# Kernel tuning notes

Measured on AMD Instinct MI355X. Metric: run time of the kernel, lower is better.

## Reference

```python
import jax, jax.numpy as jnp
import numpy as np

H = 1024        # hidden_size
V = 50257       # output_size (vocab)
L = 2048        # number of encoder annotations


def setup_inputs() -> dict:
    key = jax.random.key(0)
    ks = jax.random.split(key, 24)
    s = 0.02
    inp = {
        "input_tok": jax.random.randint(ks[0], (1,), 0, V),
        "hidden": jax.random.normal(ks[1], (1, H), jnp.float32),
        "encoder_outputs": jax.random.normal(ks[2], (L, 1, 2 * H), jnp.float32),
        "cell_state": jax.random.normal(ks[3], (1, H), jnp.float32),
        # embedding: Linear(V, H)
        "W_emb": jax.random.normal(ks[4], (V, H), jnp.float32) * s,
        "b_emb": jnp.zeros((H,), jnp.float32),
        # attn_layer: Linear(3H, H); attn_output: Linear(H, 1)
        "W_attn": jax.random.normal(ks[5], (3 * H, H), jnp.float32) * s,
        "b_attn": jnp.zeros((H,), jnp.float32),
        "W_attn_out": jax.random.normal(ks[6], (H, 1), jnp.float32) * s,
        "b_attn_out": jnp.zeros((1,), jnp.float32),
        # LSTM gates: Linear(3H + H, H) each
        "W_i": jax.random.normal(ks[7], (4 * H, H), jnp.float32) * s,
        "b_i": jnp.zeros((H,), jnp.float32),
        "W_o": jax.random.normal(ks[8], (4 * H, H), jnp.float32) * s,
        "b_o": jnp.zeros((H,), jnp.float32),
        "W_f": jax.random.normal(ks[9], (4 * H, H), jnp.float32) * s,
        "b_f": jnp.zeros((H,), jnp.float32),
        "W_c": jax.random.normal(ks[10], (4 * H, H), jnp.float32) * s,
        "b_c": jnp.zeros((H,), jnp.float32),
        # output_layer: Linear(4H, V)
        "W_out": jax.random.normal(ks[11], (4 * H, V), jnp.float32) * s,
        "b_out": jnp.zeros((V,), jnp.float32),
    }
    return inp


def reference(input_tok, hidden, encoder_outputs, cell_state,
              W_emb, b_emb, W_attn, b_attn, W_attn_out, b_attn_out,
              W_i, b_i, W_o, b_o, W_f, b_f, W_c, b_c, W_out, b_out):
    # embedding of one-hot previous token: [1, V] @ [V, H] -> [1, H]
    one_hot = jax.nn.one_hot(input_tok, V, dtype=W_emb.dtype)
    emb = one_hot @ W_emb + b_emb                     # [1, H]
    # dropout_p = 0.0 -> identity (eval-mode reference)

    enc = encoder_outputs[:, 0, :]                    # [L, 2H]
    hid_b = jnp.broadcast_to(hidden, (enc.shape[0], hidden.shape[1]))
    attn_in = jnp.concatenate([enc, hid_b], axis=1)   # [L, 3H]
    scores = jnp.tanh(attn_in @ W_attn + b_attn) @ W_attn_out + b_attn_out  # [L, 1]
    # exp(e_ij) / sum_j exp(e_ij)  ==  softmax over encoder steps
    attn_weights = jax.nn.softmax(scores, axis=0)     # [L, 1]
    context = jnp.sum(attn_weights * enc, axis=0, keepdims=True)  # [1, 2H]

    # LSTM step on cat(embedding, context) with state (hidden, cell_state)
    lstm_in = jnp.concatenate([emb, context], axis=1)              # [1, 3H]
    combined = jnp.concatenate([lstm_in, hidden], axis=1)          # [1, 4H]
    i_g = jax.nn.sigmoid(combined @ W_i + b_i)
    o_g = jax.nn.sigmoid(combined @ W_o + b_o)
    f_g = jax.nn.sigmoid(combined @ W_f + b_f)
    c_g = jnp.tanh(combined @ W_c + b_c)
    new_cell = f_g * cell_state + i_g * c_g
    next_hidden = o_g * jnp.tanh(new_cell)

    out = jnp.concatenate([emb, hidden, context], axis=1) @ W_out + b_out  # [1, V]
    log_softmax = jax.nn.log_softmax(out, axis=1)
    return (log_softmax, next_hidden, attn_weights, new_cell)
```

## Files before the change

### kernel.cpp

```cpp
#include <hip/hip_runtime.h>
#include <hip/hip_bf16.h>
#include <math.h>

#define Hh 1024
#define Vv 50257
#define Ll 2048
#define H2 2048
#define H4 4096

#define WS_EMB  0
#define WS_CTX  3072
#define WS_GATE 5120
#define WS_LOG  9216
#define WS_PAIR 59474
#define OA_BYTES 245760u
#define OB_BYTES 8634368u
#define PP 50264
#define WS_PART_F 3210240
#define WS_HBP 4014464
#define WS_SCP 4080000

#define OUT_NH Vv
#define OUT_AW (Vv + 1024)
#define OUT_NC (Vv + 3072)

typedef __attribute__((ext_vector_type(8))) short bf16x8;
typedef __attribute__((ext_vector_type(4))) float f32x4;
typedef __attribute__((ext_vector_type(4), aligned(4))) float f32x4u;

__device__ __forceinline__ float sigmoidf_(float x) { return 1.f / (1.f + expf(-x)); }
__device__ __forceinline__ unsigned short f2bf(float f) {
    union { float f; unsigned u; } v; v.f = f;
    unsigned r = v.u + 0x7FFF + ((v.u >> 16) & 1);
    return (unsigned short)(r >> 16);
}

__device__ __forceinline__ void stream_wout(const float* __restrict__ W_out,
        const float* __restrict__ xs, int k0, int v4, float* __restrict__ part_row) {
    if (v4 + 3 < Vv) {
        const char* p = (const char*)(W_out + (size_t)k0 * Vv + v4);
        const size_t st = (size_t)Vv * 4;
        f32x4 a0 = (f32x4){0.f,0.f,0.f,0.f}, a1 = a0, a2 = a0, a3 = a0;
        f32x4 a4 = a0, a5 = a0, a6 = a0, a7 = a0;
        for (int i = 0; i < 256; i += 8) {
            f32x4u w0 = __builtin_nontemporal_load((const f32x4u*)(p));
            f32x4u w1 = __builtin_nontemporal_load((const f32x4u*)(p + st));
            f32x4u w2 = __builtin_nontemporal_load((const f32x4u*)(p + 2 * st));
            f32x4u w3 = __builtin_nontemporal_load((const f32x4u*)(p + 3 * st));
            f32x4u w4 = __builtin_nontemporal_load((const f32x4u*)(p + 4 * st));
            f32x4u w5 = __builtin_nontemporal_load((const f32x4u*)(p + 5 * st));
            f32x4u w6 = __builtin_nontemporal_load((const f32x4u*)(p + 6 * st));
            f32x4u w7 = __builtin_nontemporal_load((const f32x4u*)(p + 7 * st));
            a0 += w0 * xs[i];     a1 += w1 * xs[i + 1];
            a2 += w2 * xs[i + 2]; a3 += w3 * xs[i + 3];
            a4 += w4 * xs[i + 4]; a5 += w5 * xs[i + 5];
            a6 += w6 * xs[i + 6]; a7 += w7 * xs[i + 7];
            p += 8 * st;
        }
        f32x4 a = ((a0 + a1) + (a2 + a3)) + ((a4 + a5) + (a6 + a7));
        __builtin_nontemporal_store(a, (f32x4u*)(part_row + v4));
    } else if (v4 < Vv) {
        for (int jj = 0; jj < 4 && v4 + jj < Vv; ++jj) {
            const float* p = W_out + (size_t)k0 * Vv + v4 + jj;
            float a = 0.f;
            for (int i = 0; i < 256; ++i) { a += xs[i] * (*p); p += Vv; }
            part_row[v4 + jj] = a;
        }
    }
}

__global__ __launch_bounds__(256) void kAB(const int* __restrict__ tok,
        const float* __restrict__ W_emb, const float* __restrict__ b_emb,
        const float* __restrict__ enc, const float* __restrict__ W_attn,
        const float* __restrict__ hidden, const float* __restrict__ W_out,
        float* __restrict__ ws, char* __restrict__ wsb) {
    __shared__ union { float a[16][132]; float b[32][68]; float xs[256]; } sh;
    int bx = blockIdx.x, t = threadIdx.x;
    if (bx < 250) {
        int kc = bx / 50, vb = bx % 50;
        int k0 = kc * 256;
        sh.xs[t] = (kc < 4) ? (W_emb[(size_t)tok[0] * Hh + k0 + t] + b_emb[k0 + t])
                            : hidden[k0 - 1024 + t];
        __syncthreads();
        stream_wout(W_out, sh.xs, k0, vb * 1024 + t * 4, ws + WS_PART_F + (size_t)kc * PP);
    } else if (bx < 2298) {
        int bxx = bx - 250;
        int mt = bxx >> 4, kc = bxx & 15;
        {
            int row = t >> 4, c8 = (t & 15) * 8;
            const float* src = enc + (size_t)(mt * 16 + row) * H2 + kc * 128 + c8;
            float4 v0 = *(const float4*)src;
            float4 v1 = *(const float4*)(src + 4);
            *(float4*)&sh.a[row][c8] = v0;
            *(float4*)&sh.a[row][c8 + 4] = v1;
        }
        __syncthreads();
        int ktl = t >> 6, l = t & 63;
        int r2 = l & 15, k8 = (l >> 4) * 8;
        bf16x8 o;
#pragma unroll
        for (int j = 0; j < 8; ++j) o[j] = (short)f2bf(sh.a[r2][ktl * 32 + k8 + j]);
        *(bf16x8*)(wsb + OA_BYTES + ((size_t)(mt * 64 + kc * 4 + ktl)) * 1024 + l * 16) = o;
    } else if (bx < 3322) {
        int bxx = bx - 2298;
        int kt = bxx >> 4, nc = bxx & 15;
        {
            int r = t >> 3, c8 = (t & 7) * 8;
            const float* src = W_attn + (size_t)(kt * 32 + r) * Hh + nc * 64 + c8;
            float4 v0 = *(const float4*)src;
            float4 v1 = *(const float4*)(src + 4);
            *(float4*)&sh.b[r][c8] = v0;
            *(float4*)&sh.b[r][c8 + 4] = v1;
        }
        __syncthreads();
        int ntl = t >> 6, l = t & 63;
        int col = ntl * 16 + (l & 15), k8 = (l >> 4) * 8;
        bf16x8 o;
#pragma unroll
        for (int j = 0; j < 8; ++j) o[j] = (short)f2bf(sh.b[k8 + j][col]);
        *(bf16x8*)(wsb + OB_BYTES + ((size_t)((nc * 4 + ntl) * 64 + kt)) * 1024 + l * 16) = o;
    } else if (bx < 3578) {
        int bxx = bx - 3322;
        int hc = bxx & 3, kc = bxx >> 2;
        int h = hc * 256 + t;
        int k0 = kc * 16;
        const float* p = W_attn + (size_t)(H2 + k0) * Hh + h;
        float acc = 0.f;
#pragma unroll
        for (int k = 0; k < 16; ++k) { acc += hidden[k0 + k] * __builtin_nontemporal_load(p); p += Hh; }
        ws[WS_HBP + kc * 1024 + h] = acc;
    } else {
        int i = (bx - 3578) * 256 + t;
        if (i < 1024)      ws[WS_EMB + i] = W_emb[(size_t)tok[0] * Hh + i] + b_emb[i];
        else if (i < 3072) ws[WS_CTX + (i - 1024)] = 0.f;
        else               ws[WS_GATE + (i - 3072)] = 0.f;
    }
}

__global__ __launch_bounds__(128, 1) void kC(const char* __restrict__ wsb,
        const float* __restrict__ b_attn, const float* __restrict__ Wo,
        const float* __restrict__ W_out, const float* __restrict__ hidden,
        float* __restrict__ ws) {
    __shared__ float hbv[64];
    __shared__ float xs[256];
    int bx = blockIdx.x, t = threadIdx.x;
    if (bx < 512) {
        int bm = bx >> 4, bn = bx & 15;
        int w = t >> 6, l = t & 63;
        if (t < 64) {
            int n = bn * 64 + t;
            float a = b_attn[n];
#pragma unroll 16
            for (int kc = 0; kc < 64; ++kc) a += ws[WS_HBP + kc * 1024 + n];
            hbv[t] = a;
        }
        __syncthreads();
        int mt0 = bm * 4 + w * 2;
        int nt0 = bn * 4;
        const char* pa0 = wsb + OA_BYTES + (size_t)(mt0)     * 65536 + l * 16;
        const char* pa1 = wsb + OA_BYTES + (size_t)(mt0 + 1) * 65536 + l * 16;
        const char* pb0 = wsb + OB_BYTES + (size_t)(nt0)     * 65536 + l * 16;
        const char* pb1 = wsb + OB_BYTES + (size_t)(nt0 + 1) * 65536 + l * 16;
        const char* pb2 = wsb + OB_BYTES + (size_t)(nt0 + 2) * 65536 + l * 16;
        const char* pb3 = wsb + OB_BYTES + (size_t)(nt0 + 3) * 65536 + l * 16;

        f32x4 acc[2][4];
#pragma unroll
        for (int i = 0; i < 2; ++i)
#pragma unroll
            for (int j = 0; j < 4; ++j) acc[i][j] = (f32x4){0.f, 0.f, 0.f, 0.f};

        bf16x8 As[8][2], Bs[8][4];
#define LOADK(s, kk) { int o_ = (kk) * 1024; \
    As[s][0] = *(const bf16x8*)(pa0 + o_); As[s][1] = *(const bf16x8*)(pa1 + o_); \
    Bs[s][0] = *(const bf16x8*)(pb0 + o_); Bs[s][1] = *(const bf16x8*)(pb1 + o_); \
    Bs[s][2] = *(const bf16x8*)(pb2 + o_); Bs[s][3] = *(const bf16x8*)(pb3 + o_); }
#define MFMAK(s) { \
    _Pragma("unroll") for (int mr = 0; mr < 2; ++mr) \
    _Pragma("unroll") for (int nr = 0; nr < 4; ++nr) \
        acc[mr][nr] = __builtin_amdgcn_mfma_f32_16x16x32_bf16(As[s][mr], Bs[s][nr], acc[mr][nr], 0, 0, 0); }

        LOADK(0, 0) LOADK(1, 1) LOADK(2, 2) LOADK(3, 3)
        LOADK(4, 4) LOADK(5, 5) LOADK(6, 6) LOADK(7, 7)
        for (int kt = 0; kt < 56; kt += 8) {
            MFMAK(0) LOADK(0, kt + 8)
            MFMAK(1) LOADK(1, kt + 9)
            MFMAK(2) LOADK(2, kt + 10)
            MFMAK(3) LOADK(3, kt + 11)
            MFMAK(4) LOADK(4, kt + 12)
            MFMAK(5) LOADK(5, kt + 13)
            MFMAK(6) LOADK(6, kt + 14)
            MFMAK(7) LOADK(7, kt + 15)
        }
        MFMAK(0) MFMAK(1) MFMAK(2) MFMAK(3) MFMAK(4) MFMAK(5) MFMAK(6) MFMAK(7)
#undef LOADK
#undef MFMAK

        float sp[8];
#pragma unroll
        for (int i = 0; i < 8; ++i) sp[i] = 0.f;
        int nl = l & 15;
#pragma unroll
        for (int nr = 0; nr < 4; ++nr) {
            float hb = hbv[nr * 16 + nl];
            float wo = Wo[bn * 64 + nr * 16 + nl];
#pragma unroll
            for (int mr = 0; mr < 2; ++mr)
#pragma unroll
                for (int r = 0; r < 4; ++r)
                    sp[mr * 4 + r] += tanhf(acc[mr][nr][r] + hb) * wo;
        }
#pragma unroll
        for (int m = 1; m <= 8; m <<= 1)
#pragma unroll
            for (int i = 0; i < 8; ++i) sp[i] += __shfl_xor(sp[i], m, 64);
        if ((l & 15) == 0) {
            int mbase = bm * 64 + w * 32 + (l >> 4) * 4;
#pragma unroll
            for (int mr = 0; mr < 2; ++mr)
#pragma unroll
                for (int r = 0; r < 4; ++r)
                    ws[WS_SCP + bn * 2048 + mbase + mr * 16 + r] = sp[mr * 4 + r];
        }
    } else {
        int s = bx - 512;
        int kc = 5 + s / 99, vb = s % 99;
        int k0 = kc * 256;
        xs[t] = hidden[k0 - 1024 + t];
        xs[t + 128] = hidden[k0 - 1024 + t + 128];
        __syncthreads();
        stream_wout(W_out, xs, k0, vb * 512 + t * 4, ws + WS_PART_F + (size_t)kc * PP);
    }
}

__global__ __launch_bounds__(256) void kD(const float* __restrict__ enc,
        float* __restrict__ ws, float* __restrict__ out) {
    __shared__ float red[256];
    __shared__ float wl[64];
    int bx = blockIdx.x, t = threadIdx.x;
    int jc = bx & 7, lc = bx >> 3;
    float s[8];
    float mx = -INFINITY;
#pragma unroll
    for (int i = 0; i < 8; ++i) {
        int m = i * 256 + t;
        float v = 0.f;
#pragma unroll
        for (int bn = 0; bn < 16; ++bn) v += ws[WS_SCP + bn * 2048 + m];
        s[i] = v;
        mx = fmaxf(mx, v);
    }
    red[t] = mx;
    __syncthreads();
    for (int off = 128; off > 0; off >>= 1) {
        if (t < off) red[t] = fmaxf(red[t], red[t + off]);
        __syncthreads();
    }
    float M = red[0];
    __syncthreads();
    float se = 0.f;
#pragma unroll
    for (int i = 0; i < 8; ++i) se += expf(s[i] - M);
    red[t] = se;
    __syncthreads();
    for (int off = 128; off > 0; off >>= 1) {
        if (t < off) red[t] += red[t + off];
        __syncthreads();
    }
    float invZ = 1.f / red[0];
    int l0 = lc * 64;
    if (t < 64) {
        int m = l0 + t;
        float v = 0.f;
#pragma unroll
        for (int bn = 0; bn < 16; ++bn) v += ws[WS_SCP + bn * 2048 + m];
        wl[t] = expf(v - M) * invZ;
    }
    __syncthreads();
    if (jc == 0 && t < 64) out[OUT_AW + l0 + t] = wl[t];
    int j = jc * 256 + t;
    float acc = 0.f;
#pragma unroll 8
    for (int i = 0; i < 64; ++i)
        acc += wl[i] * enc[(size_t)(l0 + i) * H2 + j];
    atomicAdd(&ws[WS_CTX + j], acc);
}

__global__ __launch_bounds__(256) void kE(const float* __restrict__ W_out,
        const float* __restrict__ W_i, const float* __restrict__ W_o,
        const float* __restrict__ W_f, const float* __restrict__ W_c,
        const float* __restrict__ hidden, float* __restrict__ ws) {
    __shared__ float xs[256];
    int bx = blockIdx.x, t = threadIdx.x;
    if (bx < 400) {
        int kc = 8 + bx / 50, vb = bx % 50;
        int k0 = kc * 256;
        xs[t] = ws[WS_CTX + k0 - 2048 + t];
        __syncthreads();
        stream_wout(W_out, xs, k0, vb * 1024 + t * 4, ws + WS_PART_F + (size_t)kc * PP);
    } else {
        int bxx = bx - 400;
        int g = bxx & 3, kc = bxx >> 2;
        int k0 = kc * 32;
        const float* Wm = (g == 0) ? W_i : (g == 1) ? W_o : (g == 2) ? W_f : W_c;
        const f32x4* p = (const f32x4*)(Wm + (size_t)k0 * Hh) + t;
        f32x4 a = (f32x4){0.f, 0.f, 0.f, 0.f};
#pragma unroll 8
        for (int k = k0; k < k0 + 32; ++k) {
            float x = (k < 1024) ? ws[WS_EMB + k] : (k < 3072) ? ws[WS_CTX + (k - 1024)] : hidden[k - 3072];
            f32x4 wv = __builtin_nontemporal_load(p);
            a += wv * x;
            p += 256;
        }
        int h4 = t * 4;
        atomicAdd(&ws[WS_GATE + g * 1024 + h4 + 0], a.x);
        atomicAdd(&ws[WS_GATE + g * 1024 + h4 + 1], a.y);
        atomicAdd(&ws[WS_GATE + g * 1024 + h4 + 2], a.z);
        atomicAdd(&ws[WS_GATE + g * 1024 + h4 + 3], a.w);
    }
}

__global__ __launch_bounds__(256) void kF(const float* __restrict__ b_i,
        const float* __restrict__ b_o, const float* __restrict__ b_f,
        const float* __restrict__ b_c, const float* __restrict__ cell,
        const float* __restrict__ b_out, float* __restrict__ ws, float* __restrict__ out) {
    int bx = blockIdx.x, t = threadIdx.x;
    if (bx < 197) {
        __shared__ float sm[256];
        int v = bx * 256 + t;
        float x = -INFINITY;
        if (v < Vv) {
            x = b_out[v];
            const float* pp = ws + WS_PART_F + v;
#pragma unroll
            for (int kc = 0; kc < 16; ++kc) x += pp[(size_t)kc * PP];
            ws[WS_LOG + v] = x;
        }
        sm[t] = x;
        __syncthreads();
        for (int off = 128; off > 0; off >>= 1) {
            if (t < off) sm[t] = fmaxf(sm[t], sm[t + off]);
            __syncthreads();
        }
        float m = sm[0];
        __syncthreads();
        sm[t] = (v < Vv) ? expf(x - m) : 0.f;
        __syncthreads();
        for (int off = 128; off > 0; off >>= 1) {
            if (t < off) sm[t] += sm[t + off];
            __syncthreads();
        }
        if (t == 0) { ws[WS_PAIR + 2 * bx] = m; ws[WS_PAIR + 2 * bx + 1] = sm[0]; }
    } else {
#pragma unroll
        for (int r = 0; r < 4; ++r) {
            int h = t + r * 256;
            float ig = sigmoidf_(ws[WS_GATE + h] + b_i[h]);
            float og = sigmoidf_(ws[WS_GATE + 1024 + h] + b_o[h]);
            float fg = sigmoidf_(ws[WS_GATE + 2048 + h] + b_f[h]);
            float cg = tanhf(ws[WS_GATE + 3072 + h] + b_c[h]);
            float nc = fg * cell[h] + ig * cg;
            out[OUT_NC + h] = nc;
            out[OUT_NH + h] = og * tanhf(nc);
        }
    }
}

__global__ __launch_bounds__(256) void k8bc(const float* __restrict__ ws, float* __restrict__ out) {
    __shared__ float sm[256], ss[256];
    int t = threadIdx.x;
    float m = (t < 197) ? ws[WS_PAIR + 2 * t] : -INFINITY;
    float s = (t < 197) ? ws[WS_PAIR + 2 * t + 1] : 0.f;
    sm[t] = m;
    __syncthreads();
    for (int off = 128; off > 0; off >>= 1) {
        if (t < off) sm[t] = fmaxf(sm[t], sm[t + off]);
        __syncthreads();
    }
    float M = sm[0];
    ss[t] = s * expf(m - M);
    __syncthreads();
    for (int off = 128; off > 0; off >>= 1) {
        if (t < off) ss[t] += ss[t + off];
        __syncthreads();
    }
    float logZ = M + logf(ss[0]);
    int v = blockIdx.x * 256 + t;
    if (v < Vv) out[v] = ws[WS_LOG + v] - logZ;
}

extern "C" void kernel_launch(void* const* d_in, const int* in_sizes, int n_in,
                              void* d_out, int out_size, void* d_ws, size_t ws_size,
                              hipStream_t stream) {
    const int*   tok        = (const int*)d_in[0];
    const float* hidden     = (const float*)d_in[1];
    const float* enc        = (const float*)d_in[2];
    const float* cell       = (const float*)d_in[3];
    const float* W_emb      = (const float*)d_in[4];
    const float* b_emb      = (const float*)d_in[5];
    const float* W_attn     = (const float*)d_in[6];
    const float* b_attn     = (const float*)d_in[7];
    const float* W_attn_out = (const float*)d_in[8];
    const float* W_i   = (const float*)d_in[10];
    const float* b_i   = (const float*)d_in[11];
    const float* W_o   = (const float*)d_in[12];
    const float* b_o   = (const float*)d_in[13];
    const float* W_f   = (const float*)d_in[14];
    const float* b_f   = (const float*)d_in[15];
    const float* W_c   = (const float*)d_in[16];
    const float* b_c   = (const float*)d_in[17];
    const float* W_out = (const float*)d_in[18];
    const float* b_out = (const float*)d_in[19];
    float* out = (float*)d_out;
    float* ws  = (float*)d_ws;
    char*  wsb = (char*)d_ws;

    kAB<<<dim3(3606), dim3(256), 0, stream>>>(tok, W_emb, b_emb, enc, W_attn, hidden, W_out, ws, wsb);
    kC<<<dim3(809), dim3(128), 0, stream>>>(wsb, b_attn, W_attn_out, W_out, hidden, ws);
    kD<<<dim3(256), dim3(256), 0, stream>>>(enc, ws, out);
    kE<<<dim3(912), dim3(256), 0, stream>>>(W_out, W_i, W_o, W_f, W_c, hidden, ws);
    kF<<<dim3(198), dim3(256), 0, stream>>>(b_i, b_o, b_f, b_c, cell, b_out, ws, out);
    k8bc<<<dim3(197), dim3(256), 0, stream>>>(ws, out);
}
```

Baseline: 240.5 us.

## Rebalance W_out streaming across kernels and replace gate atomics with partial sums

```diff
diff --git a/kernel.cpp b/kernel.cpp
--- a/kernel.cpp
+++ b/kernel.cpp
@@ -10,7 +10,6 @@
 
 #define WS_EMB  0
 #define WS_CTX  3072
-#define WS_GATE 5120
 #define WS_LOG  9216
 #define WS_PAIR 59474
 #define OA_BYTES 245760u
@@ -19,6 +18,7 @@
 #define WS_PART_F 3210240
 #define WS_HBP 4014464
 #define WS_SCP 4080000
+#define WS_GATEP 4112768
 
 #define OUT_NH Vv
 #define OUT_AW (Vv + 1024)
@@ -40,25 +40,25 @@
     if (v4 + 3 < Vv) {
         const char* p = (const char*)(W_out + (size_t)k0 * Vv + v4);
         const size_t st = (size_t)Vv * 4;
-        f32x4 a0 = (f32x4){0.f,0.f,0.f,0.f}, a1 = a0, a2 = a0, a3 = a0;
-        f32x4 a4 = a0, a5 = a0, a6 = a0, a7 = a0;
-        for (int i = 0; i < 256; i += 8) {
-            f32x4u w0 = __builtin_nontemporal_load((const f32x4u*)(p));
-            f32x4u w1 = __builtin_nontemporal_load((const f32x4u*)(p + st));
-            f32x4u w2 = __builtin_nontemporal_load((const f32x4u*)(p + 2 * st));
-            f32x4u w3 = __builtin_nontemporal_load((const f32x4u*)(p + 3 * st));
-            f32x4u w4 = __builtin_nontemporal_load((const f32x4u*)(p + 4 * st));
-            f32x4u w5 = __builtin_nontemporal_load((const f32x4u*)(p + 5 * st));
-            f32x4u w6 = __builtin_nontemporal_load((const f32x4u*)(p + 6 * st));
-            f32x4u w7 = __builtin_nontemporal_load((const f32x4u*)(p + 7 * st));
-            a0 += w0 * xs[i];     a1 += w1 * xs[i + 1];
-            a2 += w2 * xs[i + 2]; a3 += w3 * xs[i + 3];
-            a4 += w4 * xs[i + 4]; a5 += w5 * xs[i + 5];
-            a6 += w6 * xs[i + 6]; a7 += w7 * xs[i + 7];
-            p += 8 * st;
-        }
-        f32x4 a = ((a0 + a1) + (a2 + a3)) + ((a4 + a5) + (a6 + a7));
-        __builtin_nontemporal_store(a, (f32x4u*)(part_row + v4));
+        f32x4 a[16];
+#pragma unroll
+        for (int j = 0; j < 16; ++j) a[j] = (f32x4){0.f, 0.f, 0.f, 0.f};
+        for (int i = 0; i < 256; i += 16) {
+            f32x4u w[16];
+#pragma unroll
+            for (int j = 0; j < 16; ++j)
+                w[j] = __builtin_nontemporal_load((const f32x4u*)(p + (size_t)j * st));
+#pragma unroll
+            for (int j = 0; j < 16; ++j)
+                a[j] += w[j] * xs[i + j];
+            p += 16 * st;
+        }
+#pragma unroll
+        for (int off = 8; off > 0; off >>= 1)
+#pragma unroll
+            for (int j = 0; j < 8; ++j)
+                if (j < off) a[j] += a[j + off];
+        __builtin_nontemporal_store(a[0], (f32x4u*)(part_row + v4));
     } else if (v4 < Vv) {
         for (int jj = 0; jj < 4 && v4 + jj < Vv; ++jj) {
             const float* p = W_out + (size_t)k0 * Vv + v4 + jj;
@@ -69,22 +69,22 @@
     }
 }
 
-__global__ __launch_bounds__(256) void kAB(const int* __restrict__ tok,
+__global__ __launch_bounds__(256) void kP1(const int* __restrict__ tok,
         const float* __restrict__ W_emb, const float* __restrict__ b_emb,
         const float* __restrict__ enc, const float* __restrict__ W_attn,
         const float* __restrict__ hidden, const float* __restrict__ W_out,
         float* __restrict__ ws, char* __restrict__ wsb) {
     __shared__ union { float a[16][132]; float b[32][68]; float xs[256]; } sh;
     int bx = blockIdx.x, t = threadIdx.x;
-    if (bx < 250) {
+    if (bx < 400) {
         int kc = bx / 50, vb = bx % 50;
         int k0 = kc * 256;
         sh.xs[t] = (kc < 4) ? (W_emb[(size_t)tok[0] * Hh + k0 + t] + b_emb[k0 + t])
                             : hidden[k0 - 1024 + t];
         __syncthreads();
         stream_wout(W_out, sh.xs, k0, vb * 1024 + t * 4, ws + WS_PART_F + (size_t)kc * PP);
-    } else if (bx < 2298) {
-        int bxx = bx - 250;
+    } else if (bx < 2448) {
+        int bxx = bx - 400;
         int mt = bxx >> 4, kc = bxx & 15;
         {
             int row = t >> 4, c8 = (t & 15) * 8;
@@ -101,8 +101,8 @@
 #pragma unroll
         for (int j = 0; j < 8; ++j) o[j] = (short)f2bf(sh.a[r2][ktl * 32 + k8 + j]);
         *(bf16x8*)(wsb + OA_BYTES + ((size_t)(mt * 64 + kc * 4 + ktl)) * 1024 + l * 16) = o;
-    } else if (bx < 3322) {
-        int bxx = bx - 2298;
+    } else if (bx < 3472) {
+        int bxx = bx - 2448;
         int kt = bxx >> 4, nc = bxx & 15;
         {
             int r = t >> 3, c8 = (t & 7) * 8;
@@ -119,8 +119,8 @@
 #pragma unroll
         for (int j = 0; j < 8; ++j) o[j] = (short)f2bf(sh.b[k8 + j][col]);
         *(bf16x8*)(wsb + OB_BYTES + ((size_t)((nc * 4 + ntl) * 64 + kt)) * 1024 + l * 16) = o;
-    } else if (bx < 3578) {
-        int bxx = bx - 3322;
+    } else if (bx < 3728) {
+        int bxx = bx - 3472;
         int hc = bxx & 3, kc = bxx >> 2;
         int h = hc * 256 + t;
         int k0 = kc * 16;
@@ -130,47 +130,43 @@
         for (int k = 0; k < 16; ++k) { acc += hidden[k0 + k] * __builtin_nontemporal_load(p); p += Hh; }
         ws[WS_HBP + kc * 1024 + h] = acc;
     } else {
-        int i = (bx - 3578) * 256 + t;
-        if (i < 1024)      ws[WS_EMB + i] = W_emb[(size_t)tok[0] * Hh + i] + b_emb[i];
-        else if (i < 3072) ws[WS_CTX + (i - 1024)] = 0.f;
-        else               ws[WS_GATE + (i - 3072)] = 0.f;
-    }
-}
-
-__global__ __launch_bounds__(128, 1) void kC(const char* __restrict__ wsb,
+        int i = (bx - 3728) * 256 + t;
+        if (i < 1024) ws[WS_EMB + i] = W_emb[(size_t)tok[0] * Hh + i] + b_emb[i];
+        else          ws[WS_CTX + (i - 1024)] = 0.f;
+    }
+}
+
+__global__ __launch_bounds__(128, 1) void kG(const char* __restrict__ wsb,
         const float* __restrict__ b_attn, const float* __restrict__ Wo,
-        const float* __restrict__ W_out, const float* __restrict__ hidden,
         float* __restrict__ ws) {
     __shared__ float hbv[64];
-    __shared__ float xs[256];
     int bx = blockIdx.x, t = threadIdx.x;
-    if (bx < 512) {
-        int bm = bx >> 4, bn = bx & 15;
-        int w = t >> 6, l = t & 63;
-        if (t < 64) {
-            int n = bn * 64 + t;
-            float a = b_attn[n];
+    int bm = bx >> 4, bn = bx & 15;
+    int w = t >> 6, l = t & 63;
+    if (t < 64) {
+        int n = bn * 64 + t;
+        float a = b_attn[n];
 #pragma unroll 16
-            for (int kc = 0; kc < 64; ++kc) a += ws[WS_HBP + kc * 1024 + n];
-            hbv[t] = a;
-        }
-        __syncthreads();
-        int mt0 = bm * 4 + w * 2;
-        int nt0 = bn * 4;
-        const char* pa0 = wsb + OA_BYTES + (size_t)(mt0)     * 65536 + l * 16;
-        const char* pa1 = wsb + OA_BYTES + (size_t)(mt0 + 1) * 65536 + l * 16;
-        const char* pb0 = wsb + OB_BYTES + (size_t)(nt0)     * 65536 + l * 16;
-        const char* pb1 = wsb + OB_BYTES + (size_t)(nt0 + 1) * 65536 + l * 16;
-        const char* pb2 = wsb + OB_BYTES + (size_t)(nt0 + 2) * 65536 + l * 16;
-        const char* pb3 = wsb + OB_BYTES + (size_t)(nt0 + 3) * 65536 + l * 16;
-
-        f32x4 acc[2][4];
-#pragma unroll
-        for (int i = 0; i < 2; ++i)
-#pragma unroll
-            for (int j = 0; j < 4; ++j) acc[i][j] = (f32x4){0.f, 0.f, 0.f, 0.f};
-
-        bf16x8 As[8][2], Bs[8][4];
+        for (int kc = 0; kc < 64; ++kc) a += ws[WS_HBP + kc * 1024 + n];
+        hbv[t] = a;
+    }
+    __syncthreads();
+    int mt0 = bm * 4 + w * 2;
+    int nt0 = bn * 4;
+    const char* pa0 = wsb + OA_BYTES + (size_t)(mt0)     * 65536 + l * 16;
+    const char* pa1 = wsb + OA_BYTES + (size_t)(mt0 + 1) * 65536 + l * 16;
+    const char* pb0 = wsb + OB_BYTES + (size_t)(nt0)     * 65536 + l * 16;
+    const char* pb1 = wsb + OB_BYTES + (size_t)(nt0 + 1) * 65536 + l * 16;
+    const char* pb2 = wsb + OB_BYTES + (size_t)(nt0 + 2) * 65536 + l * 16;
+    const char* pb3 = wsb + OB_BYTES + (size_t)(nt0 + 3) * 65536 + l * 16;
+
+    f32x4 acc[2][4];
+#pragma unroll
+    for (int i = 0; i < 2; ++i)
+#pragma unroll
+        for (int j = 0; j < 4; ++j) acc[i][j] = (f32x4){0.f, 0.f, 0.f, 0.f};
+
+    bf16x8 As[8][2], Bs[8][4];
 #define LOADK(s, kk) { int o_ = (kk) * 1024; \
     As[s][0] = *(const bf16x8*)(pa0 + o_); As[s][1] = *(const bf16x8*)(pa1 + o_); \
     Bs[s][0] = *(const bf16x8*)(pb0 + o_); Bs[s][1] = *(const bf16x8*)(pb1 + o_); \
@@ -180,56 +176,47 @@
     _Pragma("unroll") for (int nr = 0; nr < 4; ++nr) \
         acc[mr][nr] = __builtin_amdgcn_mfma_f32_16x16x32_bf16(As[s][mr], Bs[s][nr], acc[mr][nr], 0, 0, 0); }
 
-        LOADK(0, 0) LOADK(1, 1) LOADK(2, 2) LOADK(3, 3)
-        LOADK(4, 4) LOADK(5, 5) LOADK(6, 6) LOADK(7, 7)
-        for (int kt = 0; kt < 56; kt += 8) {
-            MFMAK(0) LOADK(0, kt + 8)
-            MFMAK(1) LOADK(1, kt + 9)
-            MFMAK(2) LOADK(2, kt + 10)
-            MFMAK(3) LOADK(3, kt + 11)
-            MFMAK(4) LOADK(4, kt + 12)
-            MFMAK(5) LOADK(5, kt + 13)
-            MFMAK(6) LOADK(6, kt + 14)
-            MFMAK(7) LOADK(7, kt + 15)
-        }
-        MFMAK(0) MFMAK(1) MFMAK(2) MFMAK(3) MFMAK(4) MFMAK(5) MFMAK(6) MFMAK(7)
+    LOADK(0, 0) LOADK(1, 1) LOADK(2, 2) LOADK(3, 3)
+    LOADK(4, 4) LOADK(5, 5) LOADK(6, 6) LOADK(7, 7)
+    for (int kt = 0; kt < 56; kt += 8) {
+        MFMAK(0) LOADK(0, kt + 8)
+        MFMAK(1) LOADK(1, kt + 9)
+        MFMAK(2) LOADK(2, kt + 10)
+        MFMAK(3) LOADK(3, kt + 11)
+        MFMAK(4) LOADK(4, kt + 12)
+        MFMAK(5) LOADK(5, kt + 13)
+        MFMAK(6) LOADK(6, kt + 14)
+        MFMAK(7) LOADK(7, kt + 15)
+    }
+    MFMAK(0) MFMAK(1) MFMAK(2) MFMAK(3) MFMAK(4) MFMAK(5) MFMAK(6) MFMAK(7)
 #undef LOADK
 #undef MFMAK
 
-        float sp[8];
-#pragma unroll
-        for (int i = 0; i < 8; ++i) sp[i] = 0.f;
-        int nl = l & 15;
-#pragma unroll
-        for (int nr = 0; nr < 4; ++nr) {
-            float hb = hbv[nr * 16 + nl];
-            float wo = Wo[bn * 64 + nr * 16 + nl];
-#pragma unroll
-            for (int mr = 0; mr < 2; ++mr)
-#pragma unroll
-                for (int r = 0; r < 4; ++r)
-                    sp[mr * 4 + r] += tanhf(acc[mr][nr][r] + hb) * wo;
-        }
-#pragma unroll
-        for (int m = 1; m <= 8; m <<= 1)
-#pragma unroll
-            for (int i = 0; i < 8; ++i) sp[i] += __shfl_xor(sp[i], m, 64);
-        if ((l & 15) == 0) {
-            int mbase = bm * 64 + w * 32 + (l >> 4) * 4;
-#pragma unroll
-            for (int mr = 0; mr < 2; ++mr)
-#pragma unroll
-                for (int r = 0; r < 4; ++r)
-                    ws[WS_SCP + bn * 2048 + mbase + mr * 16 + r] = sp[mr * 4 + r];
-        }
-    } else {
-        int s = bx - 512;
-        int kc = 5 + s / 99, vb = s % 99;
-        int k0 = kc * 256;
-        xs[t] = hidden[k0 - 1024 + t];
-        xs[t + 128] = hidden[k0 - 1024 + t + 128];
-        __syncthreads();
-        stream_wout(W_out, xs, k0, vb * 512 + t * 4, ws + WS_PART_F + (size_t)kc * PP);
+    float sp[8];
+#pragma unroll
+    for (int i = 0; i < 8; ++i) sp[i] = 0.f;
+    int nl = l & 15;
+#pragma unroll
+    for (int nr = 0; nr < 4; ++nr) {
+        float hb = hbv[nr * 16 + nl];
+        float wo = Wo[bn * 64 + nr * 16 + nl];
+#pragma unroll
+        for (int mr = 0; mr < 2; ++mr)
+#pragma unroll
+            for (int r = 0; r < 4; ++r)
+                sp[mr * 4 + r] += tanhf(acc[mr][nr][r] + hb) * wo;
+    }
+#pragma unroll
+    for (int m = 1; m <= 8; m <<= 1)
+#pragma unroll
+        for (int i = 0; i < 8; ++i) sp[i] += __shfl_xor(sp[i], m, 64);
+    if ((l & 15) == 0) {
+        int mbase = bm * 64 + w * 32 + (l >> 4) * 4;
+#pragma unroll
+        for (int mr = 0; mr < 2; ++mr)
+#pragma unroll
+            for (int r = 0; r < 4; ++r)
+                ws[WS_SCP + bn * 2048 + mbase + mr * 16 + r] = sp[mr * 4 + r];
     }
 }
 
@@ -286,7 +273,7 @@
     atomicAdd(&ws[WS_CTX + j], acc);
 }
 
-__global__ __launch_bounds__(256) void kE(const float* __restrict__ W_out,
+__global__ __launch_bounds__(256) void kP2(const float* __restrict__ W_out,
         const float* __restrict__ W_i, const float* __restrict__ W_o,
         const float* __restrict__ W_f, const float* __restrict__ W_c,
         const float* __restrict__ hidden, float* __restrict__ ws) {
@@ -301,22 +288,18 @@
     } else {
         int bxx = bx - 400;
         int g = bxx & 3, kc = bxx >> 2;
-        int k0 = kc * 32;
+        int k0 = kc * 128;
         const float* Wm = (g == 0) ? W_i : (g == 1) ? W_o : (g == 2) ? W_f : W_c;
         const f32x4* p = (const f32x4*)(Wm + (size_t)k0 * Hh) + t;
         f32x4 a = (f32x4){0.f, 0.f, 0.f, 0.f};
 #pragma unroll 8
-        for (int k = k0; k < k0 + 32; ++k) {
+        for (int k = k0; k < k0 + 128; ++k) {
             float x = (k < 1024) ? ws[WS_EMB + k] : (k < 3072) ? ws[WS_CTX + (k - 1024)] : hidden[k - 3072];
             f32x4 wv = __builtin_nontemporal_load(p);
             a += wv * x;
             p += 256;
         }
-        int h4 = t * 4;
-        atomicAdd(&ws[WS_GATE + g * 1024 + h4 + 0], a.x);
-        atomicAdd(&ws[WS_GATE + g * 1024 + h4 + 1], a.y);
-        atomicAdd(&ws[WS_GATE + g * 1024 + h4 + 2], a.z);
-        atomicAdd(&ws[WS_GATE + g * 1024 + h4 + 3], a.w);
+        *(f32x4*)&ws[WS_GATEP + (size_t)(g * 32 + kc) * 1024 + t * 4] = a;
     }
 }
 
@@ -355,10 +338,19 @@
 #pragma unroll
         for (int r = 0; r < 4; ++r) {
             int h = t + r * 256;
-            float ig = sigmoidf_(ws[WS_GATE + h] + b_i[h]);
-            float og = sigmoidf_(ws[WS_GATE + 1024 + h] + b_o[h]);
-            float fg = sigmoidf_(ws[WS_GATE + 2048 + h] + b_f[h]);
-            float cg = tanhf(ws[WS_GATE + 3072 + h] + b_c[h]);
+            float gp[4];
+#pragma unroll
+            for (int g = 0; g < 4; ++g) {
+                float s = 0.f;
+#pragma unroll 8
+                for (int kc = 0; kc < 32; ++kc)
+                    s += ws[WS_GATEP + (size_t)(g * 32 + kc) * 1024 + h];
+                gp[g] = s;
+            }
+            float ig = sigmoidf_(gp[0] + b_i[h]);
+            float og = sigmoidf_(gp[1] + b_o[h]);
+            float fg = sigmoidf_(gp[2] + b_f[h]);
+            float cg = tanhf(gp[3] + b_c[h]);
             float nc = fg * cell[h] + ig * cg;
             out[OUT_NC + h] = nc;
             out[OUT_NH + h] = og * tanhf(nc);
@@ -415,10 +407,10 @@
     float* ws  = (float*)d_ws;
     char*  wsb = (char*)d_ws;
 
-    kAB<<<dim3(3606), dim3(256), 0, stream>>>(tok, W_emb, b_emb, enc, W_attn, hidden, W_out, ws, wsb);
-    kC<<<dim3(809), dim3(128), 0, stream>>>(wsb, b_attn, W_attn_out, W_out, hidden, ws);
+    kP1<<<dim3(3740), dim3(256), 0, stream>>>(tok, W_emb, b_emb, enc, W_attn, hidden, W_out, ws, wsb);
+    kG<<<dim3(512), dim3(128), 0, stream>>>(wsb, b_attn, W_attn_out, ws);
     kD<<<dim3(256), dim3(256), 0, stream>>>(enc, ws, out);
-    kE<<<dim3(912), dim3(256), 0, stream>>>(W_out, W_i, W_o, W_f, W_c, hidden, ws);
+    kP2<<<dim3(528), dim3(256), 0, stream>>>(W_out, W_i, W_o, W_f, W_c, hidden, ws);
     kF<<<dim3(198), dim3(256), 0, stream>>>(b_i, b_o, b_f, b_c, cell, b_out, ws, out);
     k8bc<<<dim3(197), dim3(256), 0, stream>>>(ws, out);
 }
```

Result: slower. 289.2 us (+20.2%).
